# Kernel optimization log

Measured on AMD Instinct MI355X. Metric: run time of the kernel, lower is better.

Reference implementation:

```python
import jax, jax.numpy as jnp
import numpy as np

B, S, D = 2, 2048, 1024
H = 16
HD = D // H

def setup_inputs() -> dict:
    key = jax.random.key(0)
    k1, k2, k3 = jax.random.split(key, 3)
    x = jax.random.normal(k1, (B, S, D), dtype=jnp.float32)
    w_attn = jax.random.normal(k2, (D, 3 * D), dtype=jnp.float32) * (1.0 / np.sqrt(D))
    b_attn = jnp.zeros((3 * D,), dtype=jnp.float32)
    w_proj = jax.random.normal(k3, (D, D), dtype=jnp.float32) * (1.0 / np.sqrt(D))
    b_proj = jnp.zeros((D,), dtype=jnp.float32)
    return {"x": x, "w_attn": w_attn, "b_attn": b_attn, "w_proj": w_proj, "b_proj": b_proj}

def reference(x, w_attn, b_attn, w_proj, b_proj):
    bsz, seq_len, embed_dim = x.shape
    qkv = x @ w_attn + b_attn                      # [B,S,3D]
    q, k, v = jnp.split(qkv, 3, axis=-1)
    # [B,S,D] -> [B,H,S,HD]
    def heads(t):
        return t.reshape(bsz, seq_len, H, HD).transpose(0, 2, 1, 3)
    q, k, v = heads(q), heads(k), heads(v)
    scale = 1.0 / np.sqrt(HD)
    att = jnp.einsum('bhqd,bhkd->bhqk', q, k) * scale  # [B,H,S,S]
    causal = jnp.tril(jnp.ones((seq_len, seq_len), dtype=bool))
    att = jnp.where(causal[None, None], att, jnp.float32(-jnp.inf))
    att = jax.nn.softmax(att, axis=-1)
    y = jnp.einsum('bhqk,bhkd->bhqd', att, v)          # [B,H,S,HD]
    y = y.transpose(0, 2, 1, 3).reshape(bsz, seq_len, embed_dim)
    return y @ w_proj + b_proj
```

## Files before the change

kernel.cpp:

```cpp
#include <hip/hip_runtime.h>
#include <hip/hip_bf16.h>
#include <math.h>

typedef __bf16 bf16x8 __attribute__((ext_vector_type(8)));
typedef __bf16 bf16x4 __attribute__((ext_vector_type(4)));
typedef float f32x4 __attribute__((ext_vector_type(4)));

#define LOG2E 1.44269504088896340736f

#define SEQ 2048
#define DMODEL 1024
#define NH 16
#define HD 64

__device__ __forceinline__ void gl2lds16(const void* g, void* l) {
  __builtin_amdgcn_global_load_lds((__attribute__((address_space(1))) void*)g,
                                   (__attribute__((address_space(3))) void*)l,
                                   16, 0, 0);
}

__global__ void detect_dtype(const unsigned* __restrict__ x, unsigned* __restrict__ flag) {
  __shared__ int cnt[256];
  int c = 0;
  for (int i = threadIdx.x; i < 4096; i += 256) {
    unsigned e = (x[i] >> 23) & 0xFF;
    c += (e >= 0x70 && e <= 0x8F) ? 1 : 0;
  }
  cnt[threadIdx.x] = c;
  __syncthreads();
  for (int s = 128; s > 0; s >>= 1) {
    if ((int)threadIdx.x < s) cnt[threadIdx.x] += cnt[threadIdx.x + s];
    __syncthreads();
  }
  if (threadIdx.x == 0) flag[0] = (cnt[0] > 2048) ? 1u : 0u;
}

__global__ void conv_to_bf16(const void* __restrict__ in, __hip_bfloat16* __restrict__ out,
                             int n, const unsigned* __restrict__ flag) {
  const int i = (blockIdx.x * 256 + threadIdx.x) * 4;
  if (i >= n) return;
  if (*flag) {
    const float4 v = *(const float4*)((const float*)in + i);
    out[i + 0] = __float2bfloat16(v.x);
    out[i + 1] = __float2bfloat16(v.y);
    out[i + 2] = __float2bfloat16(v.z);
    out[i + 3] = __float2bfloat16(v.w);
  } else {
    const __hip_bfloat16* bin = (const __hip_bfloat16*)in;
    out[i + 0] = bin[i + 0];
    out[i + 1] = bin[i + 1];
    out[i + 2] = bin[i + 2];
    out[i + 3] = bin[i + 3];
  }
}

__global__ void transpose_cvt(const void* __restrict__ in, __hip_bfloat16* __restrict__ out,
                              int R, int C, const unsigned* __restrict__ flag) {
  __shared__ __hip_bfloat16 tile[64][65];
  const bool f32 = (*flag != 0);
  const int c0 = blockIdx.x * 64, r0 = blockIdx.y * 64;
  const int tx = threadIdx.x & 63, ty = threadIdx.x >> 6;
#pragma unroll
  for (int i = 0; i < 16; ++i) {
    int r = ty + i * 4;
    long idx = (long)(r0 + r) * C + c0 + tx;
    tile[r][tx] = f32 ? __float2bfloat16(((const float*)in)[idx])
                      : ((const __hip_bfloat16*)in)[idx];
  }
  __syncthreads();
#pragma unroll
  for (int i = 0; i < 16; ++i) {
    int r = ty + i * 4;
    out[(long)(c0 + r) * R + r0 + tx] = tile[tx][r];
  }
}

template <int MODE>
__global__ __launch_bounds__(256, 2) void gemm_bt(
    const __hip_bfloat16* __restrict__ A, const __hip_bfloat16* __restrict__ Bt,
    const __hip_bfloat16* __restrict__ bias, void* __restrict__ C,
    __hip_bfloat16* __restrict__ q_ws, __hip_bfloat16* __restrict__ k_ws,
    __hip_bfloat16* __restrict__ vt_ws, int M, int N, int K,
    const unsigned* __restrict__ flag) {
  alignas(16) __shared__ __hip_bfloat16 lA[128 * 32];
  alignas(16) __shared__ __hip_bfloat16 lB[128 * 32];
  const int tid = threadIdx.x;
  const int wave = tid >> 6, lane = tid & 63;
  const int l15 = lane & 15, lq = lane >> 4;
  const int m0 = blockIdx.y * 128, n0 = blockIdx.x * 128;
  const int wrow = (wave >> 1) * 64, wcol = (wave & 1) * 64;

  const __hip_bfloat16* ap0 = A + (long)(m0 + wave * 16 + (lane >> 2)) * K + (lane & 3) * 8;
  const __hip_bfloat16* bp0 = Bt + (long)(n0 + wave * 16 + (lane >> 2)) * K + (lane & 3) * 8;
  __hip_bfloat16* lA0 = lA + wave * 512;
  __hip_bfloat16* lA1 = lA + (wave + 4) * 512;
  __hip_bfloat16* lB0 = lB + wave * 512;
  __hip_bfloat16* lB1 = lB + (wave + 4) * 512;

  f32x4 acc[4][4];
#pragma unroll
  for (int i = 0; i < 4; ++i)
#pragma unroll
    for (int j = 0; j < 4; ++j) acc[i][j] = {0.f, 0.f, 0.f, 0.f};

  for (int k0 = 0; k0 < K; k0 += 32) {
    __syncthreads();
    gl2lds16(ap0 + k0, lA0);
    gl2lds16(ap0 + (long)64 * K + k0, lA1);
    gl2lds16(bp0 + k0, lB0);
    gl2lds16(bp0 + (long)64 * K + k0, lB1);
    __syncthreads();
    bf16x8 af[4], bfr[4];
#pragma unroll
    for (int i = 0; i < 4; ++i)
      af[i] = *(const bf16x8*)(lA + (wrow + 16 * i + l15) * 32 + lq * 8);
#pragma unroll
    for (int j = 0; j < 4; ++j)
      bfr[j] = *(const bf16x8*)(lB + (wcol + 16 * j + l15) * 32 + lq * 8);
#pragma unroll
    for (int i = 0; i < 4; ++i)
#pragma unroll
      for (int j = 0; j < 4; ++j)
        acc[i][j] = __builtin_amdgcn_mfma_f32_16x16x32_bf16(af[i], bfr[j], acc[i][j], 0, 0, 0);
  }

  const bool outf32 = (MODE == 0) && (*flag != 0);
#pragma unroll
  for (int i = 0; i < 4; ++i) {
    const int row = m0 + wrow + 16 * i + lq * 4;
#pragma unroll
    for (int j = 0; j < 4; ++j) {
      const int col = n0 + wcol + 16 * j + l15;
      const float bv = __bfloat162float(bias[col]);
#pragma unroll
      for (int r = 0; r < 4; ++r) {
        const float v = acc[i][j][r] + bv;
        const int rr = row + r;
        if (MODE == 0) {
          if (outf32)
            ((float*)C)[(long)rr * N + col] = v;
          else
            ((__hip_bfloat16*)C)[(long)rr * N + col] = __float2bfloat16(v);
        } else {
          const int which = col >> 10;
          const int f = col & 1023;
          const int h = f >> 6, d = f & 63;
          const int b = rr >> 11, s = rr & 2047;
          const long bh = (long)b * NH + h;
          const __hip_bfloat16 hv = __float2bfloat16(v);
          if (which == 0)
            q_ws[(bh * SEQ + s) * HD + d] = hv;
          else if (which == 1)
            k_ws[(bh * SEQ + s) * HD + d] = hv;
          else {
            const int w = s & 31;
            const int wl = w & 15;
            const int sig = (w >> 4) ? (2 * (wl & ~3) + 4 + (wl & 3))
                                     : (2 * (wl & ~3) + (wl & 3));
            const int sp = (s & ~31) | sig;
            vt_ws[(bh * HD + d) * SEQ + sp] = hv;
          }
        }
      }
    }
  }
}

__global__ __launch_bounds__(256, 4) void attn_fused(
    const __hip_bfloat16* __restrict__ q_ws, const __hip_bfloat16* __restrict__ k_ws,
    const __hip_bfloat16* __restrict__ vt_ws, __hip_bfloat16* __restrict__ y_ws) {
  alignas(16) __shared__ __hip_bfloat16 lK[2][64 * 64];
  alignas(16) __shared__ __hip_bfloat16 lV[2][64 * 64];
  const int tid = threadIdx.x, wave = tid >> 6, lane = tid & 63;
  const int l15 = lane & 15, lq = lane >> 4;
  const int qt = 31 - (blockIdx.x >> 5);
  const int bh = blockIdx.x & 31;
  const int q0 = qt * 64;
  const int nkt = qt + 1;
  const __hip_bfloat16* Qb = q_ws + (long)bh * SEQ * HD;
  const __hip_bfloat16* Kb = k_ws + (long)bh * SEQ * HD;
  const __hip_bfloat16* Vb = vt_ws + (long)bh * HD * SEQ;
  const int b = bh >> 4, h = bh & 15;
  const float SCL = 0.125f * LOG2E;

  const int qrow = q0 + wave * 16 + l15;
  const bf16x8 qa0 = *(const bf16x8*)(Qb + (long)qrow * HD + lq * 8);
  const bf16x8 qa1 = *(const bf16x8*)(Qb + (long)qrow * HD + 32 + lq * 8);

  f32x4 accO[4];
#pragma unroll
  for (int j = 0; j < 4; ++j) accO[j] = {0.f, 0.f, 0.f, 0.f};
  float l_part = 0.f;

  const int p0 = wave * 16 + (lane >> 3);
  const int cl = lane & 7;

#pragma unroll
  for (int i = 0; i < 2; ++i) {
    const int p = p0 + i * 8;
    const int c = cl ^ (p & 7);
    gl2lds16(Kb + (long)p * HD + c * 8, &lK[0][(wave * 16 + i * 8) * 64]);
    gl2lds16(Vb + (long)p * SEQ + c * 8, &lV[0][(wave * 16 + i * 8) * 64]);
  }
  __syncthreads();

#pragma unroll 1
  for (int kt = 0; kt < nkt; ++kt) {
    const int buf = kt & 1;
    if (kt + 1 < nkt) {
      const int kb = (kt + 1) * 64;
#pragma unroll
      for (int i = 0; i < 2; ++i) {
        const int p = p0 + i * 8;
        const int c = cl ^ (p & 7);
        gl2lds16(Kb + (long)(kb + p) * HD + c * 8, &lK[buf ^ 1][(wave * 16 + i * 8) * 64]);
        gl2lds16(Vb + (long)p * SEQ + kb + c * 8, &lV[buf ^ 1][(wave * 16 + i * 8) * 64]);
      }
    }
    const __hip_bfloat16* lKb = lK[buf];
    const __hip_bfloat16* lVb = lV[buf];

    f32x4 st[4];
#pragma unroll
    for (int t = 0; t < 4; ++t) {
      st[t] = {0.f, 0.f, 0.f, 0.f};
      const int pp = t * 16 + l15;
      const bf16x8 kb0 = *(const bf16x8*)(lKb + (pp * 8 + (lq ^ (pp & 7))) * 8);
      const bf16x8 kb1 = *(const bf16x8*)(lKb + (pp * 8 + ((4 + lq) ^ (pp & 7))) * 8);
      st[t] = __builtin_amdgcn_mfma_f32_16x16x32_bf16(kb0, qa0, st[t], 0, 0, 0);
      st[t] = __builtin_amdgcn_mfma_f32_16x16x32_bf16(kb1, qa1, st[t], 0, 0, 0);
    }

    const bool diag = (kt == nkt - 1);
    const int qloc = wave * 16 + l15;
    bf16x8 pb[2];
#pragma unroll
    for (int c = 0; c < 2; ++c) {
#pragma unroll
      for (int t2 = 0; t2 < 2; ++t2) {
        const int tt = c * 2 + t2;
#pragma unroll
        for (int r = 0; r < 4; ++r) {
          float pv = exp2f(st[tt][r] * SCL);
          if (diag) {
            const int colloc = tt * 16 + lq * 4 + r;
            pv = (colloc <= qloc) ? pv : 0.f;
          }
          l_part += pv;
          pb[c][t2 * 4 + r] = (__bf16)pv;
        }
      }
    }

#pragma unroll
    for (int j = 0; j < 4; ++j) {
      const int d = j * 16 + l15;
      const bf16x8 va0 = *(const bf16x8*)(lVb + (d * 8 + (lq ^ (d & 7))) * 8);
      const bf16x8 va1 = *(const bf16x8*)(lVb + (d * 8 + ((4 + lq) ^ (d & 7))) * 8);
      accO[j] = __builtin_amdgcn_mfma_f32_16x16x32_bf16(va0, pb[0], accO[j], 0, 0, 0);
      accO[j] = __builtin_amdgcn_mfma_f32_16x16x32_bf16(va1, pb[1], accO[j], 0, 0, 0);
    }
    __syncthreads();
  }

  float l = l_part;
  l += __shfl_xor(l, 16, 64);
  l += __shfl_xor(l, 32, 64);
  const float inv = 1.f / l;
  const int s = q0 + wave * 16 + l15;
  __hip_bfloat16* yb = y_ws + (long)(b * SEQ + s) * DMODEL + h * HD;
#pragma unroll
  for (int j = 0; j < 4; ++j) {
    bf16x4 o;
#pragma unroll
    for (int r = 0; r < 4; ++r) o[r] = (__bf16)(accO[j][r] * inv);
    *(bf16x4*)(yb + j * 16 + lq * 4) = o;
  }
}

extern "C" void kernel_launch(void* const* d_in, const int* in_sizes, int n_in,
                              void* d_out, int out_size, void* d_ws, size_t ws_size,
                              hipStream_t stream) {
  const void* x = d_in[0];
  const void* w_attn = d_in[1];
  const void* b_attn = d_in[2];
  const void* w_proj = d_in[3];
  const void* b_proj = d_in[4];

  char* ws = (char*)d_ws;
  const size_t MB = 1024 * 1024;
  unsigned* flag = (unsigned*)ws;
  __hip_bfloat16* wT_attn = (__hip_bfloat16*)(ws + 1 * MB);
  __hip_bfloat16* wT_proj = (__hip_bfloat16*)(ws + 7 * MB);
  __hip_bfloat16* x_bf = (__hip_bfloat16*)(ws + 9 * MB);
  __hip_bfloat16* q_ws = (__hip_bfloat16*)(ws + 17 * MB);
  __hip_bfloat16* k_ws = (__hip_bfloat16*)(ws + 25 * MB);
  __hip_bfloat16* vt_ws = (__hip_bfloat16*)(ws + 33 * MB);
  __hip_bfloat16* y_ws = (__hip_bfloat16*)(ws + 41 * MB);
  __hip_bfloat16* bA_bf = (__hip_bfloat16*)(ws + 49 * MB);
  __hip_bfloat16* bP_bf = (__hip_bfloat16*)(ws + 49 * MB + 8192);

  detect_dtype<<<1, 256, 0, stream>>>((const unsigned*)x, flag);

  conv_to_bf16<<<4096, 256, 0, stream>>>(x, x_bf, 4194304, flag);
  conv_to_bf16<<<3, 256, 0, stream>>>(b_attn, bA_bf, 3072, flag);
  conv_to_bf16<<<1, 256, 0, stream>>>(b_proj, bP_bf, 1024, flag);
  transpose_cvt<<<dim3(3072 / 64, 1024 / 64), 256, 0, stream>>>(w_attn, wT_attn, 1024, 3072, flag);
  transpose_cvt<<<dim3(1024 / 64, 1024 / 64), 256, 0, stream>>>(w_proj, wT_proj, 1024, 1024, flag);

  gemm_bt<1><<<dim3(3072 / 128, 4096 / 128), 256, 0, stream>>>(
      x_bf, wT_attn, bA_bf, nullptr, q_ws, k_ws, vt_ws, 4096, 3072, 1024, flag);

  attn_fused<<<dim3(1024), 256, 0, stream>>>(q_ws, k_ws, vt_ws, y_ws);

  gemm_bt<0><<<dim3(1024 / 128, 4096 / 128), 256, 0, stream>>>(
      y_ws, wT_proj, bP_bf, d_out, nullptr, nullptr, nullptr, 4096, 1024, 1024, flag);
}
```

Measured before the change: 213.1 us.

## Swizzle GEMM LDS, raise occupancy, fold softmax scale into K, MFMA row sums

The GEMM now XOR-swizzles the 16-byte column chunks on the global-to-LDS load and on the fragment reads, to cut LDS bank conflicts, and its launch bound goes from 2 to 4 blocks per CU. The softmax scale times log2(e) is applied to K when the QKV GEMM writes it, which removes a multiply per score in attention. The per-row softmax denominator is now accumulated with an MFMA against a ones vector, replacing scalar adds and cross-lane shuffles. Risks are register spilling under the tighter launch bound and rounding differences from scaling K before its bf16 conversion.

Result: faster. 207.2 us (-2.8%).

```diff
diff --git a/kernel.cpp b/kernel.cpp
--- a/kernel.cpp
+++ b/kernel.cpp
@@ -76,7 +76,7 @@
 }
 
 template <int MODE>
-__global__ __launch_bounds__(256, 2) void gemm_bt(
+__global__ __launch_bounds__(256, 4) void gemm_bt(
     const __hip_bfloat16* __restrict__ A, const __hip_bfloat16* __restrict__ Bt,
     const __hip_bfloat16* __restrict__ bias, void* __restrict__ C,
     __hip_bfloat16* __restrict__ q_ws, __hip_bfloat16* __restrict__ k_ws,
@@ -90,8 +90,9 @@
   const int m0 = blockIdx.y * 128, n0 = blockIdx.x * 128;
   const int wrow = (wave >> 1) * 64, wcol = (wave & 1) * 64;
 
-  const __hip_bfloat16* ap0 = A + (long)(m0 + wave * 16 + (lane >> 2)) * K + (lane & 3) * 8;
-  const __hip_bfloat16* bp0 = Bt + (long)(n0 + wave * 16 + (lane >> 2)) * K + (lane & 3) * 8;
+  const int cg = (lane & 3) ^ ((lane >> 3) & 3);
+  const __hip_bfloat16* ap0 = A + (long)(m0 + wave * 16 + (lane >> 2)) * K + cg * 8;
+  const __hip_bfloat16* bp0 = Bt + (long)(n0 + wave * 16 + (lane >> 2)) * K + cg * 8;
   __hip_bfloat16* lA0 = lA + wave * 512;
   __hip_bfloat16* lA1 = lA + (wave + 4) * 512;
   __hip_bfloat16* lB0 = lB + wave * 512;
@@ -102,6 +103,8 @@
   for (int i = 0; i < 4; ++i)
 #pragma unroll
     for (int j = 0; j < 4; ++j) acc[i][j] = {0.f, 0.f, 0.f, 0.f};
+
+  const int fc = (lq ^ ((l15 >> 1) & 3)) * 8;
 
   for (int k0 = 0; k0 < K; k0 += 32) {
     __syncthreads();
@@ -113,10 +116,10 @@
     bf16x8 af[4], bfr[4];
 #pragma unroll
     for (int i = 0; i < 4; ++i)
-      af[i] = *(const bf16x8*)(lA + (wrow + 16 * i + l15) * 32 + lq * 8);
+      af[i] = *(const bf16x8*)(lA + (wrow + 16 * i + l15) * 32 + fc);
 #pragma unroll
     for (int j = 0; j < 4; ++j)
-      bfr[j] = *(const bf16x8*)(lB + (wcol + 16 * j + l15) * 32 + lq * 8);
+      bfr[j] = *(const bf16x8*)(lB + (wcol + 16 * j + l15) * 32 + fc);
 #pragma unroll
     for (int i = 0; i < 4; ++i)
 #pragma unroll
@@ -125,6 +128,7 @@
   }
 
   const bool outf32 = (MODE == 0) && (*flag != 0);
+  const float KSCL = 0.125f * LOG2E;
 #pragma unroll
   for (int i = 0; i < 4; ++i) {
     const int row = m0 + wrow + 16 * i + lq * 4;
@@ -147,18 +151,17 @@
           const int h = f >> 6, d = f & 63;
           const int b = rr >> 11, s = rr & 2047;
           const long bh = (long)b * NH + h;
-          const __hip_bfloat16 hv = __float2bfloat16(v);
           if (which == 0)
-            q_ws[(bh * SEQ + s) * HD + d] = hv;
+            q_ws[(bh * SEQ + s) * HD + d] = __float2bfloat16(v);
           else if (which == 1)
-            k_ws[(bh * SEQ + s) * HD + d] = hv;
+            k_ws[(bh * SEQ + s) * HD + d] = __float2bfloat16(v * KSCL);
           else {
             const int w = s & 31;
             const int wl = w & 15;
             const int sig = (w >> 4) ? (2 * (wl & ~3) + 4 + (wl & 3))
                                      : (2 * (wl & ~3) + (wl & 3));
             const int sp = (s & ~31) | sig;
-            vt_ws[(bh * HD + d) * SEQ + sp] = hv;
+            vt_ws[(bh * HD + d) * SEQ + sp] = __float2bfloat16(v);
           }
         }
       }
@@ -181,16 +184,18 @@
   const __hip_bfloat16* Kb = k_ws + (long)bh * SEQ * HD;
   const __hip_bfloat16* Vb = vt_ws + (long)bh * HD * SEQ;
   const int b = bh >> 4, h = bh & 15;
-  const float SCL = 0.125f * LOG2E;
 
   const int qrow = q0 + wave * 16 + l15;
   const bf16x8 qa0 = *(const bf16x8*)(Qb + (long)qrow * HD + lq * 8);
   const bf16x8 qa1 = *(const bf16x8*)(Qb + (long)qrow * HD + 32 + lq * 8);
 
   f32x4 accO[4];
+  f32x4 accL;
 #pragma unroll
   for (int j = 0; j < 4; ++j) accO[j] = {0.f, 0.f, 0.f, 0.f};
-  float l_part = 0.f;
+  accL = {0.f, 0.f, 0.f, 0.f};
+  const __bf16 one = (__bf16)1.0f;
+  const bf16x8 onesA = {one, one, one, one, one, one, one, one};
 
   const int p0 = wave * 16 + (lane >> 3);
   const int cl = lane & 7;
@@ -241,12 +246,11 @@
         const int tt = c * 2 + t2;
 #pragma unroll
         for (int r = 0; r < 4; ++r) {
-          float pv = exp2f(st[tt][r] * SCL);
+          float pv = exp2f(st[tt][r]);
           if (diag) {
             const int colloc = tt * 16 + lq * 4 + r;
             pv = (colloc <= qloc) ? pv : 0.f;
           }
-          l_part += pv;
           pb[c][t2 * 4 + r] = (__bf16)pv;
         }
       }
@@ -260,13 +264,12 @@
       accO[j] = __builtin_amdgcn_mfma_f32_16x16x32_bf16(va0, pb[0], accO[j], 0, 0, 0);
       accO[j] = __builtin_amdgcn_mfma_f32_16x16x32_bf16(va1, pb[1], accO[j], 0, 0, 0);
     }
+    accL = __builtin_amdgcn_mfma_f32_16x16x32_bf16(onesA, pb[0], accL, 0, 0, 0);
+    accL = __builtin_amdgcn_mfma_f32_16x16x32_bf16(onesA, pb[1], accL, 0, 0, 0);
     __syncthreads();
   }
 
-  float l = l_part;
-  l += __shfl_xor(l, 16, 64);
-  l += __shfl_xor(l, 32, 64);
-  const float inv = 1.f / l;
+  const float inv = 1.f / accL[0];
   const int s = q0 + wave * 16 + l15;
   __hip_bfloat16* yb = y_ws + (long)(b * SEQ + s) * DMODEL + h * HD;
 #pragma unroll
```
